# Performance work log

Measured on AMD Instinct MI355X. Metric: run time of the kernel, lower is better.

The kernel has to match this reference:

```python
import jax, jax.numpy as jnp
import numpy as np

B, LQ, LK, D = 32, 2048, 2048, 64


def setup_inputs() -> dict:
    key = jax.random.key(0)
    k1, k2, k3, k4 = jax.random.split(key, 4)
    querys = jax.random.normal(k1, (B, LQ, D), dtype=jnp.float32)
    keys = jax.random.normal(k2, (B, LK, D), dtype=jnp.float32)
    values = jax.random.normal(k3, (B, LK, D), dtype=jnp.float32)
    # valid lengths in [1, LK]
    valid_lens = jax.random.randint(k4, (B,), 1, LK + 1, dtype=jnp.int32)
    return {"querys": querys, "keys": keys, "values": values, "valid_lens": valid_lens}


def reference(querys, keys, values, valid_lens):
    d = querys.shape[-1]
    # [B, Lq, Lk] score matrix
    scores = jnp.einsum("bqd,bkd->bqk", querys, keys) / jnp.sqrt(jnp.asarray(d, querys.dtype))
    # masked softmax: key positions >= valid_len get -1e6 (as in d2l masked_softmax)
    key_pos = jnp.arange(scores.shape[-1], dtype=jnp.int32)  # [Lk]
    mask = key_pos[None, None, :] < valid_lens[:, None, None]  # [B, 1, Lk]
    scores = jnp.where(mask, scores, jnp.asarray(-1e6, scores.dtype))
    attn = jax.nn.softmax(scores, axis=-1)
    # dropout p=0.0 -> identity
    return jnp.einsum("bqk,bkd->bqd", attn, values)
```

## Files before the change

### kernel.cpp

```cpp
#include <hip/hip_runtime.h>
#include <hip/hip_bf16.h>
#include <math.h>


#define B_    32
#define LQ_   2048
#define LK_   2048
#define D_    64

typedef __attribute__((ext_vector_type(8)))  short bf16x8;
typedef __attribute__((ext_vector_type(4)))  float f32x4;
typedef __attribute__((ext_vector_type(16))) float f32x16;

static __device__ __forceinline__ unsigned pk_bf16(float a, float b) {
    __hip_bfloat162 h = __float22bfloat162_rn(float2{a, b});
    return *(unsigned*)&h;
}

__global__ __launch_bounds__(128, 2) void fa_mfma3_kernel(
    const float* __restrict__ Q, const float* __restrict__ K,
    const float* __restrict__ V, const int* __restrict__ vlen,
    float* __restrict__ O)
{
    __shared__ __align__(16) short Kl[2][64 * 64];
    __shared__ __align__(16) short Vt[2][64 * 64];

    const int tid  = threadIdx.x;
    const int wave = tid >> 6;
    const int lane = tid & 63;
    const int c31  = lane & 31;
    const int h    = lane >> 5;

    const int b  = blockIdx.y;
    const int q0 = blockIdx.x * 64 + wave * 32;
    const int vl = vlen[b];
    const int nt = (vl + 63) >> 6;

    const float qscale = 0.125f * 1.44269504088896340736f;

    unsigned qfrag[4][4];
#pragma unroll
    for (int ks = 0; ks < 4; ++ks) {
        const float* qp = Q + ((size_t)(b * LQ_ + q0 + c31)) * D_ + ks * 16 + h * 8;
        f32x4 t0 = *(const f32x4*)qp;
        f32x4 t1 = *(const f32x4*)(qp + 4);
#pragma unroll
        for (int jj = 0; jj < 2; ++jj) {
            qfrag[ks][jj]     = pk_bf16(t0[2*jj] * qscale, t0[2*jj+1] * qscale);
            qfrag[ks][jj + 2] = pk_bf16(t1[2*jj] * qscale, t1[2*jj+1] * qscale);
        }
    }

    f32x16 oacc[2];
#pragma unroll
    for (int dt = 0; dt < 2; ++dt)
#pragma unroll
        for (int r = 0; r < 16; ++r) oacc[dt][r] = 0.f;
    float mrun = -INFINITY, lrun = 0.f;

    const int skey = tid >> 1, skh = tid & 1;
    const int vkg = tid >> 4, vdg = tid & 15;

    const float* kgp = K + ((size_t)(b * LK_ + skey)) * D_ + skh * 32;
    const float* vgp = V + ((size_t)(b * LK_ + vkg * 8)) * D_ + vdg * 4;

    f32x4 kr[8], vr[8];
#pragma unroll
    for (int i = 0; i < 8; ++i) kr[i] = *(const f32x4*)(kgp + 4 * i);
#pragma unroll
    for (int i = 0; i < 8; ++i) vr[i] = *(const f32x4*)(vgp + (size_t)i * D_);

    for (int t = 0; t < nt; ++t) {
        const int k0 = t * 64;
        const int buf = t & 1;

        {
            unsigned pk32[16];
#pragma unroll
            for (int m = 0; m < 16; ++m)
                pk32[m] = pk_bf16(kr[m >> 1][2 * (m & 1)], kr[m >> 1][2 * (m & 1) + 1]);
#pragma unroll
            for (int cch = 0; cch < 4; ++cch) {
                const int pos = (skh * 4 + cch) ^ (skey & 7);
                *(bf16x8*)&Kl[buf][skey * 64 + pos * 8] = *(bf16x8*)&pk32[4 * cch];
            }
#pragma unroll
            for (int dr = 0; dr < 4; ++dr) {
                unsigned w[4];
#pragma unroll
                for (int p = 0; p < 4; ++p)
                    w[p] = pk_bf16(vr[2 * p][dr], vr[2 * p + 1][dr]);
                const int dim = vdg * 4 + dr;
                const int pos = vkg ^ (dim & 7);
                *(bf16x8*)&Vt[buf][dim * 64 + pos * 8] = *(bf16x8*)&w[0];
            }
        }
        if (t + 1 < nt) {
            const float* kn = kgp + (size_t)(k0 + 64) * D_;
            const float* vn = vgp + (size_t)(k0 + 64) * D_;
#pragma unroll
            for (int i = 0; i < 8; ++i) kr[i] = *(const f32x4*)(kn + 4 * i);
#pragma unroll
            for (int i = 0; i < 8; ++i) vr[i] = *(const f32x4*)(vn + (size_t)i * D_);
        }
        __syncthreads();

        f32x16 st[2];
#pragma unroll
        for (int s = 0; s < 2; ++s) {
#pragma unroll
            for (int r = 0; r < 16; ++r) st[s][r] = 0.f;
#pragma unroll
            for (int ks = 0; ks < 4; ++ks) {
                const int pos = (ks * 2 + h) ^ (c31 & 7);
                bf16x8 kf = *(const bf16x8*)&Kl[buf][(s * 32 + c31) * 64 + pos * 8];
                st[s] = __builtin_amdgcn_mfma_f32_32x32x16_bf16(
                    kf, *(const bf16x8*)&qfrag[ks][0], st[s], 0, 0, 0);
            }
        }

        if (k0 + 64 > vl) {
#pragma unroll
            for (int s = 0; s < 2; ++s) {
                const int base = k0 + s * 32 + 4 * h;
#pragma unroll
                for (int r = 0; r < 16; ++r) {
                    const int key = base + (r & 3) + 8 * (r >> 2);
                    if (key >= vl) st[s][r] = -1e30f;
                }
            }
        }

        float tm = st[0][0];
#pragma unroll
        for (int s = 0; s < 2; ++s)
#pragma unroll
            for (int r = 0; r < 16; ++r) tm = fmaxf(tm, st[s][r]);
        tm = fmaxf(tm, __shfl_xor(tm, 32));
        const float mnew = fmaxf(mrun, tm);
        const float corr = exp2f(mrun - mnew);
        mrun = mnew;
        float rs = 0.f;
#pragma unroll
        for (int s = 0; s < 2; ++s)
#pragma unroll
            for (int r = 0; r < 16; ++r) {
                const float p = exp2f(st[s][r] - mnew);
                st[s][r] = p;
                rs += p;
            }
        rs += __shfl_xor(rs, 32);
        lrun = lrun * corr + rs;
#pragma unroll
        for (int dt = 0; dt < 2; ++dt)
#pragma unroll
            for (int r = 0; r < 16; ++r) oacc[dt][r] *= corr;

        unsigned pk[2][8];
#pragma unroll
        for (int s = 0; s < 2; ++s)
#pragma unroll
            for (int m = 0; m < 8; ++m)
                pk[s][m] = pk_bf16(st[s][2 * m], st[s][2 * m + 1]);

#pragma unroll
        for (int kq = 0; kq < 4; ++kq) {
            const int s = kq >> 1, A4 = (kq & 1) * 4;
            unsigned p0 = pk[s][A4], p1 = pk[s][A4+1], p2 = pk[s][A4+2], p3 = pk[s][A4+3];
            unsigned xp0 = __shfl_xor((int)p0, 32);
            unsigned xp1 = __shfl_xor((int)p1, 32);
            unsigned xp2 = __shfl_xor((int)p2, 32);
            unsigned xp3 = __shfl_xor((int)p3, 32);
            unsigned pf[4];
            pf[0] = h ? xp2 : p0;
            pf[1] = h ? xp3 : p1;
            pf[2] = h ? p2  : xp0;
            pf[3] = h ? p3  : xp1;
            const bf16x8 pfr = *(const bf16x8*)&pf[0];
#pragma unroll
            for (int dt = 0; dt < 2; ++dt) {
                const int pos = (kq * 2 + h) ^ (c31 & 7);
                bf16x8 vf = *(const bf16x8*)&Vt[buf][(dt * 32 + c31) * 64 + pos * 8];
                oacc[dt] = __builtin_amdgcn_mfma_f32_32x32x16_bf16(vf, pfr, oacc[dt], 0, 0, 0);
            }
        }
    }

    const float inv = 1.f / lrun;
    float* op = O + ((size_t)(b * LQ_ + q0 + c31)) * D_;
#pragma unroll
    for (int dt = 0; dt < 2; ++dt)
#pragma unroll
        for (int g = 0; g < 4; ++g) {
            f32x4 v;
#pragma unroll
            for (int j = 0; j < 4; ++j) v[j] = oacc[dt][4 * g + j] * inv;
            *(f32x4*)(op + dt * 32 + 8 * g + 4 * h) = v;
        }
}

extern "C" void kernel_launch(void* const* d_in, const int* in_sizes, int n_in,
                              void* d_out, int out_size, void* d_ws, size_t ws_size,
                              hipStream_t stream) {
    const float* Q    = (const float*)d_in[0];
    const float* K    = (const float*)d_in[1];
    const float* V    = (const float*)d_in[2];
    const int*   vlen = (const int*)d_in[3];
    float*       O    = (float*)d_out;

    dim3 grid(LQ_ / 64, B_);
    dim3 block(128);
    fa_mfma3_kernel<<<grid, block, 0, stream>>>(Q, K, V, vlen, O);
}
```

Baseline: 171.1 us.

## Split key range across two wave groups per block and add lazy rescaling

Doubles the block to 256 threads, splitting the key tiles between two groups of waves that each handle alternating 64-key tiles into their own double-buffered LDS. The two partial softmax states are merged through shared memory at the end. Separately, the running max is updated only when a new tile max exceeds it by more than 8 (log2 domain), which skips the rescale of the accumulators most of the time. The cost is twice the LDS per block, a final cross-group reduction, extra barriers, and a lazy-rescale scheme whose bounded overflow margin must hold.

```diff
diff --git a/kernel.cpp b/kernel.cpp
--- a/kernel.cpp
+++ b/kernel.cpp
@@ -17,24 +17,28 @@
     return *(unsigned*)&h;
 }
 
-__global__ __launch_bounds__(128, 2) void fa_mfma3_kernel(
+__global__ __launch_bounds__(256, 2) void fa_mfma5_kernel(
     const float* __restrict__ Q, const float* __restrict__ K,
     const float* __restrict__ V, const int* __restrict__ vlen,
     float* __restrict__ O)
 {
-    __shared__ __align__(16) short Kl[2][64 * 64];
-    __shared__ __align__(16) short Vt[2][64 * 64];
+    __shared__ __align__(16) short Kl[2][2][64 * 64];
+    __shared__ __align__(16) short Vt[2][2][64 * 64];
 
     const int tid  = threadIdx.x;
-    const int wave = tid >> 6;
+    const int wid  = tid >> 6;
+    const int grp  = wid >> 1;
+    const int wsub = wid & 1;
     const int lane = tid & 63;
     const int c31  = lane & 31;
     const int h    = lane >> 5;
+    const int ltid = tid & 127;
 
     const int b  = blockIdx.y;
-    const int q0 = blockIdx.x * 64 + wave * 32;
+    const int q0 = blockIdx.x * 64 + wsub * 32;
     const int vl = vlen[b];
     const int nt = (vl + 63) >> 6;
+    const int ni = (nt + 1) >> 1;
 
     const float qscale = 0.125f * 1.44269504088896340736f;
 
@@ -58,23 +62,28 @@
         for (int r = 0; r < 16; ++r) oacc[dt][r] = 0.f;
     float mrun = -INFINITY, lrun = 0.f;
 
-    const int skey = tid >> 1, skh = tid & 1;
-    const int vkg = tid >> 4, vdg = tid & 15;
+    const int skey = ltid >> 1, skh = ltid & 1;
+    const int vkg = ltid >> 4, vdg = ltid & 15;
 
     const float* kgp = K + ((size_t)(b * LK_ + skey)) * D_ + skh * 32;
     const float* vgp = V + ((size_t)(b * LK_ + vkg * 8)) * D_ + vdg * 4;
 
     f32x4 kr[8], vr[8];
-#pragma unroll
-    for (int i = 0; i < 8; ++i) kr[i] = *(const f32x4*)(kgp + 4 * i);
-#pragma unroll
-    for (int i = 0; i < 8; ++i) vr[i] = *(const f32x4*)(vgp + (size_t)i * D_);
-
-    for (int t = 0; t < nt; ++t) {
-        const int k0 = t * 64;
-        const int buf = t & 1;
-
-        {
+    {
+        const size_t off = (size_t)(grp * 64) * D_;
+#pragma unroll
+        for (int i = 0; i < 8; ++i) kr[i] = *(const f32x4*)(kgp + off + 4 * i);
+#pragma unroll
+        for (int i = 0; i < 8; ++i) vr[i] = *(const f32x4*)(vgp + off + (size_t)i * D_);
+    }
+
+    for (int it = 0; it < ni; ++it) {
+        const int t   = 2 * it + grp;
+        const int k0  = t * 64;
+        const int buf = it & 1;
+        const bool active = (t < nt);
+
+        if (active) {
             unsigned pk32[16];
 #pragma unroll
             for (int m = 0; m < 16; ++m)
@@ -82,7 +91,7 @@
 #pragma unroll
             for (int cch = 0; cch < 4; ++cch) {
                 const int pos = (skh * 4 + cch) ^ (skey & 7);
-                *(bf16x8*)&Kl[buf][skey * 64 + pos * 8] = *(bf16x8*)&pk32[4 * cch];
+                *(bf16x8*)&Kl[grp][buf][skey * 64 + pos * 8] = *(bf16x8*)&pk32[4 * cch];
             }
 #pragma unroll
             for (int dr = 0; dr < 4; ++dr) {
@@ -92,18 +101,19 @@
                     w[p] = pk_bf16(vr[2 * p][dr], vr[2 * p + 1][dr]);
                 const int dim = vdg * 4 + dr;
                 const int pos = vkg ^ (dim & 7);
-                *(bf16x8*)&Vt[buf][dim * 64 + pos * 8] = *(bf16x8*)&w[0];
-            }
-        }
-        if (t + 1 < nt) {
-            const float* kn = kgp + (size_t)(k0 + 64) * D_;
-            const float* vn = vgp + (size_t)(k0 + 64) * D_;
+                *(bf16x8*)&Vt[grp][buf][dim * 64 + pos * 8] = *(bf16x8*)&w[0];
+            }
+        }
+        if (t + 2 < nt) {
+            const float* kn = kgp + (size_t)(k0 + 128) * D_;
+            const float* vn = vgp + (size_t)(k0 + 128) * D_;
 #pragma unroll
             for (int i = 0; i < 8; ++i) kr[i] = *(const f32x4*)(kn + 4 * i);
 #pragma unroll
             for (int i = 0; i < 8; ++i) vr[i] = *(const f32x4*)(vn + (size_t)i * D_);
         }
         __syncthreads();
+        if (!active) continue;
 
         f32x16 st[2];
 #pragma unroll
@@ -113,7 +123,7 @@
 #pragma unroll
             for (int ks = 0; ks < 4; ++ks) {
                 const int pos = (ks * 2 + h) ^ (c31 & 7);
-                bf16x8 kf = *(const bf16x8*)&Kl[buf][(s * 32 + c31) * 64 + pos * 8];
+                bf16x8 kf = *(const bf16x8*)&Kl[grp][buf][(s * 32 + c31) * 64 + pos * 8];
                 st[s] = __builtin_amdgcn_mfma_f32_32x32x16_bf16(
                     kf, *(const bf16x8*)&qfrag[ks][0], st[s], 0, 0, 0);
             }
@@ -137,24 +147,27 @@
 #pragma unroll
             for (int r = 0; r < 16; ++r) tm = fmaxf(tm, st[s][r]);
         tm = fmaxf(tm, __shfl_xor(tm, 32));
-        const float mnew = fmaxf(mrun, tm);
-        const float corr = exp2f(mrun - mnew);
-        mrun = mnew;
+        if (__any(tm > mrun + 8.f)) {
+            const float mnew = fmaxf(mrun, tm);
+            const float corr = exp2f(mrun - mnew);
+            lrun *= corr;
+#pragma unroll
+            for (int dt = 0; dt < 2; ++dt)
+#pragma unroll
+                for (int r = 0; r < 16; ++r) oacc[dt][r] *= corr;
+            mrun = mnew;
+        }
         float rs = 0.f;
 #pragma unroll
         for (int s = 0; s < 2; ++s)
 #pragma unroll
             for (int r = 0; r < 16; ++r) {
-                const float p = exp2f(st[s][r] - mnew);
+                const float p = exp2f(st[s][r] - mrun);
                 st[s][r] = p;
                 rs += p;
             }
         rs += __shfl_xor(rs, 32);
-        lrun = lrun * corr + rs;
-#pragma unroll
-        for (int dt = 0; dt < 2; ++dt)
-#pragma unroll
-            for (int r = 0; r < 16; ++r) oacc[dt][r] *= corr;
+        lrun += rs;
 
         unsigned pk[2][8];
 #pragma unroll
@@ -180,23 +193,52 @@
 #pragma unroll
             for (int dt = 0; dt < 2; ++dt) {
                 const int pos = (kq * 2 + h) ^ (c31 & 7);
-                bf16x8 vf = *(const bf16x8*)&Vt[buf][(dt * 32 + c31) * 64 + pos * 8];
+                bf16x8 vf = *(const bf16x8*)&Vt[grp][buf][(dt * 32 + c31) * 64 + pos * 8];
                 oacc[dt] = __builtin_amdgcn_mfma_f32_32x32x16_bf16(vf, pfr, oacc[dt], 0, 0, 0);
             }
         }
     }
 
-    const float inv = 1.f / lrun;
-    float* op = O + ((size_t)(b * LQ_ + q0 + c31)) * D_;
-#pragma unroll
-    for (int dt = 0; dt < 2; ++dt)
-#pragma unroll
-        for (int g = 0; g < 4; ++g) {
-            f32x4 v;
-#pragma unroll
-            for (int j = 0; j < 4; ++j) v[j] = oacc[dt][4 * g + j] * inv;
-            *(f32x4*)(op + dt * 32 + 8 * g + 4 * h) = v;
-        }
+    __syncthreads();
+
+    float* xO = (float*)&Kl[1][0][0];
+    float* xM = (float*)&Vt[1][0][0];
+    if (grp == 1) {
+#pragma unroll
+        for (int dt = 0; dt < 2; ++dt)
+#pragma unroll
+            for (int r = 0; r < 16; ++r) {
+                const int dim = dt * 32 + (r & 3) + 8 * (r >> 2) + 4 * h;
+                xO[wsub * 2048 + dim * 32 + c31] = oacc[dt][r];
+            }
+        if (h == 0) {
+            xM[wsub * 64 + c31]      = mrun;
+            xM[wsub * 64 + 32 + c31] = lrun;
+        }
+    }
+    __syncthreads();
+    if (grp == 0) {
+        const float m1 = xM[wsub * 64 + c31];
+        const float l1 = xM[wsub * 64 + 32 + c31];
+        const float mf = fmaxf(mrun, m1);
+        const float c0 = exp2f(mrun - mf);
+        const float c1 = exp2f(m1 - mf);
+        const float inv = 1.f / (lrun * c0 + l1 * c1);
+        float* op = O + ((size_t)(b * LQ_ + q0 + c31)) * D_;
+#pragma unroll
+        for (int dt = 0; dt < 2; ++dt)
+#pragma unroll
+            for (int g = 0; g < 4; ++g) {
+                f32x4 v;
+#pragma unroll
+                for (int j = 0; j < 4; ++j) {
+                    const int dim = dt * 32 + 8 * g + 4 * h + j;
+                    v[j] = (oacc[dt][4 * g + j] * c0 +
+                            xO[wsub * 2048 + dim * 32 + c31] * c1) * inv;
+                }
+                *(f32x4*)(op + dt * 32 + 8 * g + 4 * h) = v;
+            }
+    }
 }
 
 extern "C" void kernel_launch(void* const* d_in, const int* in_sizes, int n_in,
@@ -209,6 +251,6 @@
     float*       O    = (float*)d_out;
 
     dim3 grid(LQ_ / 64, B_);
-    dim3 block(128);
-    fa_mfma3_kernel<<<grid, block, 0, stream>>>(Q, K, V, vlen, O);
+    dim3 block(256);
+    fa_mfma5_kernel<<<grid, block, 0, stream>>>(Q, K, V, vlen, O);
 }
```

After: 171.9 us. Within noise of the previous version (+0.5%).

## Split key dimension across blocks with merge kernel and lazy rescale

Applied to the files above, without the earlier changes.

Splits each batch's key range into up to four chunks processed by separate blocks, writing partial outputs and (max, sum) stats to workspace, then merges them in a second kernel. The aim is to even out load imbalance from variable valid lengths and raise occupancy. It also adds a lazy online-softmax rescale that only updates the running max when it grows by more than 8 (log2 units). In exchange it adds substantial partial-output write and read traffic plus a second launch, and a monolithic fallback is kept for when no workspace is available.

```diff
diff --git a/kernel.cpp b/kernel.cpp
--- a/kernel.cpp
+++ b/kernel.cpp
@@ -17,10 +17,10 @@
     return *(unsigned*)&h;
 }
 
-__global__ __launch_bounds__(128, 2) void fa_mfma3_kernel(
+__global__ __launch_bounds__(128, 2) void fa_split_kernel(
     const float* __restrict__ Q, const float* __restrict__ K,
     const float* __restrict__ V, const int* __restrict__ vlen,
-    float* __restrict__ O)
+    float* __restrict__ OP, float* __restrict__ ML)
 {
     __shared__ __align__(16) short Kl[2][64 * 64];
     __shared__ __align__(16) short Vt[2][64 * 64];
@@ -32,9 +32,14 @@
     const int h    = lane >> 5;
 
     const int b  = blockIdx.y;
+    const int s  = blockIdx.z;
+    const int NS = gridDim.z;
     const int q0 = blockIdx.x * 64 + wave * 32;
     const int vl = vlen[b];
-    const int nt = (vl + 63) >> 6;
+    const int nt    = (vl + 63) >> 6;
+    const int chunk = (nt + NS - 1) / NS;
+    const int t0    = s * chunk;
+    const int t1    = min(t0 + chunk, nt);
 
     const float qscale = 0.125f * 1.44269504088896340736f;
 
@@ -42,12 +47,12 @@
 #pragma unroll
     for (int ks = 0; ks < 4; ++ks) {
         const float* qp = Q + ((size_t)(b * LQ_ + q0 + c31)) * D_ + ks * 16 + h * 8;
-        f32x4 t0 = *(const f32x4*)qp;
-        f32x4 t1 = *(const f32x4*)(qp + 4);
+        f32x4 t0v = *(const f32x4*)qp;
+        f32x4 t1v = *(const f32x4*)(qp + 4);
 #pragma unroll
         for (int jj = 0; jj < 2; ++jj) {
-            qfrag[ks][jj]     = pk_bf16(t0[2*jj] * qscale, t0[2*jj+1] * qscale);
-            qfrag[ks][jj + 2] = pk_bf16(t1[2*jj] * qscale, t1[2*jj+1] * qscale);
+            qfrag[ks][jj]     = pk_bf16(t0v[2*jj] * qscale, t0v[2*jj+1] * qscale);
+            qfrag[ks][jj + 2] = pk_bf16(t1v[2*jj] * qscale, t1v[2*jj+1] * qscale);
         }
     }
 
@@ -65,12 +70,15 @@
     const float* vgp = V + ((size_t)(b * LK_ + vkg * 8)) * D_ + vdg * 4;
 
     f32x4 kr[8], vr[8];
-#pragma unroll
-    for (int i = 0; i < 8; ++i) kr[i] = *(const f32x4*)(kgp + 4 * i);
-#pragma unroll
-    for (int i = 0; i < 8; ++i) vr[i] = *(const f32x4*)(vgp + (size_t)i * D_);
-
-    for (int t = 0; t < nt; ++t) {
+    if (t0 < t1) {
+        const size_t off = (size_t)t0 * 64 * D_;
+#pragma unroll
+        for (int i = 0; i < 8; ++i) kr[i] = *(const f32x4*)(kgp + off + 4 * i);
+#pragma unroll
+        for (int i = 0; i < 8; ++i) vr[i] = *(const f32x4*)(vgp + off + (size_t)i * D_);
+    }
+
+    for (int t = t0; t < t1; ++t) {
         const int k0 = t * 64;
         const int buf = t & 1;
 
@@ -95,7 +103,7 @@
                 *(bf16x8*)&Vt[buf][dim * 64 + pos * 8] = *(bf16x8*)&w[0];
             }
         }
-        if (t + 1 < nt) {
+        if (t + 1 < t1) {
             const float* kn = kgp + (size_t)(k0 + 64) * D_;
             const float* vn = vgp + (size_t)(k0 + 64) * D_;
 #pragma unroll
@@ -107,66 +115,69 @@
 
         f32x16 st[2];
 #pragma unroll
-        for (int s = 0; s < 2; ++s) {
-#pragma unroll
-            for (int r = 0; r < 16; ++r) st[s][r] = 0.f;
+        for (int ss = 0; ss < 2; ++ss) {
+#pragma unroll
+            for (int r = 0; r < 16; ++r) st[ss][r] = 0.f;
 #pragma unroll
             for (int ks = 0; ks < 4; ++ks) {
                 const int pos = (ks * 2 + h) ^ (c31 & 7);
-                bf16x8 kf = *(const bf16x8*)&Kl[buf][(s * 32 + c31) * 64 + pos * 8];
-                st[s] = __builtin_amdgcn_mfma_f32_32x32x16_bf16(
-                    kf, *(const bf16x8*)&qfrag[ks][0], st[s], 0, 0, 0);
+                bf16x8 kf = *(const bf16x8*)&Kl[buf][(ss * 32 + c31) * 64 + pos * 8];
+                st[ss] = __builtin_amdgcn_mfma_f32_32x32x16_bf16(
+                    kf, *(const bf16x8*)&qfrag[ks][0], st[ss], 0, 0, 0);
             }
         }
 
         if (k0 + 64 > vl) {
 #pragma unroll
-            for (int s = 0; s < 2; ++s) {
-                const int base = k0 + s * 32 + 4 * h;
+            for (int ss = 0; ss < 2; ++ss) {
+                const int base = k0 + ss * 32 + 4 * h;
 #pragma unroll
                 for (int r = 0; r < 16; ++r) {
                     const int key = base + (r & 3) + 8 * (r >> 2);
-                    if (key >= vl) st[s][r] = -1e30f;
+                    if (key >= vl) st[ss][r] = -1e30f;
                 }
             }
         }
 
         float tm = st[0][0];
 #pragma unroll
-        for (int s = 0; s < 2; ++s)
-#pragma unroll
-            for (int r = 0; r < 16; ++r) tm = fmaxf(tm, st[s][r]);
+        for (int ss = 0; ss < 2; ++ss)
+#pragma unroll
+            for (int r = 0; r < 16; ++r) tm = fmaxf(tm, st[ss][r]);
         tm = fmaxf(tm, __shfl_xor(tm, 32));
-        const float mnew = fmaxf(mrun, tm);
-        const float corr = exp2f(mrun - mnew);
-        mrun = mnew;
+        if (__any(tm > mrun + 8.f)) {
+            const float mnew = fmaxf(mrun, tm);
+            const float corr = exp2f(mrun - mnew);
+            lrun *= corr;
+#pragma unroll
+            for (int dt = 0; dt < 2; ++dt)
+#pragma unroll
+                for (int r = 0; r < 16; ++r) oacc[dt][r] *= corr;
+            mrun = mnew;
+        }
         float rs = 0.f;
 #pragma unroll
-        for (int s = 0; s < 2; ++s)
+        for (int ss = 0; ss < 2; ++ss)
 #pragma unroll
             for (int r = 0; r < 16; ++r) {
-                const float p = exp2f(st[s][r] - mnew);
-                st[s][r] = p;
+                const float p = exp2f(st[ss][r] - mrun);
+                st[ss][r] = p;
                 rs += p;
             }
         rs += __shfl_xor(rs, 32);
-        lrun = lrun * corr + rs;
-#pragma unroll
-        for (int dt = 0; dt < 2; ++dt)
-#pragma unroll
-            for (int r = 0; r < 16; ++r) oacc[dt][r] *= corr;
+        lrun += rs;
 
         unsigned pk[2][8];
 #pragma unroll
-        for (int s = 0; s < 2; ++s)
+        for (int ss = 0; ss < 2; ++ss)
 #pragma unroll
             for (int m = 0; m < 8; ++m)
-                pk[s][m] = pk_bf16(st[s][2 * m], st[s][2 * m + 1]);
+                pk[ss][m] = pk_bf16(st[ss][2 * m], st[ss][2 * m + 1]);
 
 #pragma unroll
         for (int kq = 0; kq < 4; ++kq) {
-            const int s = kq >> 1, A4 = (kq & 1) * 4;
-            unsigned p0 = pk[s][A4], p1 = pk[s][A4+1], p2 = pk[s][A4+2], p3 = pk[s][A4+3];
+            const int ss = kq >> 1, A4 = (kq & 1) * 4;
+            unsigned p0 = pk[ss][A4], p1 = pk[ss][A4+1], p2 = pk[ss][A4+2], p3 = pk[ss][A4+3];
             unsigned xp0 = __shfl_xor((int)p0, 32);
             unsigned xp1 = __shfl_xor((int)p1, 32);
             unsigned xp2 = __shfl_xor((int)p2, 32);
@@ -186,6 +197,219 @@
         }
     }
 
+    const size_t row = (size_t)s * (B_ * LQ_) + b * LQ_ + q0 + c31;
+    float* op = OP + row * D_;
+#pragma unroll
+    for (int dt = 0; dt < 2; ++dt)
+#pragma unroll
+        for (int g = 0; g < 4; ++g) {
+            f32x4 v;
+#pragma unroll
+            for (int j = 0; j < 4; ++j) v[j] = oacc[dt][4 * g + j];
+            *(f32x4*)(op + dt * 32 + 8 * g + 4 * h) = v;
+        }
+    if (h == 0)
+        *(float2*)&ML[row * 2] = float2{mrun, lrun};
+}
+
+template<int NS>
+__global__ __launch_bounds__(256) void fa_merge_kernel(
+    const float* __restrict__ OP, const float* __restrict__ ML,
+    float* __restrict__ O)
+{
+    const int g   = blockIdx.x * 256 + threadIdx.x;
+    const int row = g >> 4;
+    const int qd  = (g & 15) * 4;
+
+    float mf = -INFINITY;
+#pragma unroll
+    for (int s = 0; s < NS; ++s) {
+        float2 ml = *(const float2*)&ML[((size_t)s * (B_ * LQ_) + row) * 2];
+        mf = fmaxf(mf, ml.x);
+    }
+    float den = 0.f;
+    f32x4 acc = {0.f, 0.f, 0.f, 0.f};
+#pragma unroll
+    for (int s = 0; s < NS; ++s) {
+        const size_t srow = (size_t)s * (B_ * LQ_) + row;
+        float2 ml = *(const float2*)&ML[srow * 2];
+        const float c = exp2f(ml.x - mf);
+        den += c * ml.y;
+        f32x4 v = *(const f32x4*)&OP[srow * D_ + qd];
+        acc += v * c;
+    }
+    const float inv = 1.f / den;
+    *(f32x4*)(O + (size_t)row * D_ + qd) = acc * inv;
+}
+
+__global__ __launch_bounds__(128, 2) void fa_mono_kernel(
+    const float* __restrict__ Q, const float* __restrict__ K,
+    const float* __restrict__ V, const int* __restrict__ vlen,
+    float* __restrict__ O)
+{
+    __shared__ __align__(16) short Kl[2][64 * 64];
+    __shared__ __align__(16) short Vt[2][64 * 64];
+
+    const int tid  = threadIdx.x;
+    const int wave = tid >> 6;
+    const int lane = tid & 63;
+    const int c31  = lane & 31;
+    const int h    = lane >> 5;
+
+    const int b  = blockIdx.y;
+    const int q0 = blockIdx.x * 64 + wave * 32;
+    const int vl = vlen[b];
+    const int nt = (vl + 63) >> 6;
+
+    const float qscale = 0.125f * 1.44269504088896340736f;
+
+    unsigned qfrag[4][4];
+#pragma unroll
+    for (int ks = 0; ks < 4; ++ks) {
+        const float* qp = Q + ((size_t)(b * LQ_ + q0 + c31)) * D_ + ks * 16 + h * 8;
+        f32x4 t0 = *(const f32x4*)qp;
+        f32x4 t1 = *(const f32x4*)(qp + 4);
+#pragma unroll
+        for (int jj = 0; jj < 2; ++jj) {
+            qfrag[ks][jj]     = pk_bf16(t0[2*jj] * qscale, t0[2*jj+1] * qscale);
+            qfrag[ks][jj + 2] = pk_bf16(t1[2*jj] * qscale, t1[2*jj+1] * qscale);
+        }
+    }
+
+    f32x16 oacc[2];
+#pragma unroll
+    for (int dt = 0; dt < 2; ++dt)
+#pragma unroll
+        for (int r = 0; r < 16; ++r) oacc[dt][r] = 0.f;
+    float mrun = -INFINITY, lrun = 0.f;
+
+    const int skey = tid >> 1, skh = tid & 1;
+    const int vkg = tid >> 4, vdg = tid & 15;
+
+    const float* kgp = K + ((size_t)(b * LK_ + skey)) * D_ + skh * 32;
+    const float* vgp = V + ((size_t)(b * LK_ + vkg * 8)) * D_ + vdg * 4;
+
+    f32x4 kr[8], vr[8];
+#pragma unroll
+    for (int i = 0; i < 8; ++i) kr[i] = *(const f32x4*)(kgp + 4 * i);
+#pragma unroll
+    for (int i = 0; i < 8; ++i) vr[i] = *(const f32x4*)(vgp + (size_t)i * D_);
+
+    for (int t = 0; t < nt; ++t) {
+        const int k0 = t * 64;
+        const int buf = t & 1;
+        {
+            unsigned pk32[16];
+#pragma unroll
+            for (int m = 0; m < 16; ++m)
+                pk32[m] = pk_bf16(kr[m >> 1][2 * (m & 1)], kr[m >> 1][2 * (m & 1) + 1]);
+#pragma unroll
+            for (int cch = 0; cch < 4; ++cch) {
+                const int pos = (skh * 4 + cch) ^ (skey & 7);
+                *(bf16x8*)&Kl[buf][skey * 64 + pos * 8] = *(bf16x8*)&pk32[4 * cch];
+            }
+#pragma unroll
+            for (int dr = 0; dr < 4; ++dr) {
+                unsigned w[4];
+#pragma unroll
+                for (int p = 0; p < 4; ++p)
+                    w[p] = pk_bf16(vr[2 * p][dr], vr[2 * p + 1][dr]);
+                const int dim = vdg * 4 + dr;
+                const int pos = vkg ^ (dim & 7);
+                *(bf16x8*)&Vt[buf][dim * 64 + pos * 8] = *(bf16x8*)&w[0];
+            }
+        }
+        if (t + 1 < nt) {
+            const float* kn = kgp + (size_t)(k0 + 64) * D_;
+            const float* vn = vgp + (size_t)(k0 + 64) * D_;
+#pragma unroll
+            for (int i = 0; i < 8; ++i) kr[i] = *(const f32x4*)(kn + 4 * i);
+#pragma unroll
+            for (int i = 0; i < 8; ++i) vr[i] = *(const f32x4*)(vn + (size_t)i * D_);
+        }
+        __syncthreads();
+
+        f32x16 st[2];
+#pragma unroll
+        for (int ss = 0; ss < 2; ++ss) {
+#pragma unroll
+            for (int r = 0; r < 16; ++r) st[ss][r] = 0.f;
+#pragma unroll
+            for (int ks = 0; ks < 4; ++ks) {
+                const int pos = (ks * 2 + h) ^ (c31 & 7);
+                bf16x8 kf = *(const bf16x8*)&Kl[buf][(ss * 32 + c31) * 64 + pos * 8];
+                st[ss] = __builtin_amdgcn_mfma_f32_32x32x16_bf16(
+                    kf, *(const bf16x8*)&qfrag[ks][0], st[ss], 0, 0, 0);
+            }
+        }
+        if (k0 + 64 > vl) {
+#pragma unroll
+            for (int ss = 0; ss < 2; ++ss) {
+                const int base = k0 + ss * 32 + 4 * h;
+#pragma unroll
+                for (int r = 0; r < 16; ++r) {
+                    const int key = base + (r & 3) + 8 * (r >> 2);
+                    if (key >= vl) st[ss][r] = -1e30f;
+                }
+            }
+        }
+        float tm = st[0][0];
+#pragma unroll
+        for (int ss = 0; ss < 2; ++ss)
+#pragma unroll
+            for (int r = 0; r < 16; ++r) tm = fmaxf(tm, st[ss][r]);
+        tm = fmaxf(tm, __shfl_xor(tm, 32));
+        if (__any(tm > mrun + 8.f)) {
+            const float mnew = fmaxf(mrun, tm);
+            const float corr = exp2f(mrun - mnew);
+            lrun *= corr;
+#pragma unroll
+            for (int dt = 0; dt < 2; ++dt)
+#pragma unroll
+                for (int r = 0; r < 16; ++r) oacc[dt][r] *= corr;
+            mrun = mnew;
+        }
+        float rs = 0.f;
+#pragma unroll
+        for (int ss = 0; ss < 2; ++ss)
+#pragma unroll
+            for (int r = 0; r < 16; ++r) {
+                const float p = exp2f(st[ss][r] - mrun);
+                st[ss][r] = p;
+                rs += p;
+            }
+        rs += __shfl_xor(rs, 32);
+        lrun += rs;
+
+        unsigned pk[2][8];
+#pragma unroll
+        for (int ss = 0; ss < 2; ++ss)
+#pragma unroll
+            for (int m = 0; m < 8; ++m)
+                pk[ss][m] = pk_bf16(st[ss][2 * m], st[ss][2 * m + 1]);
+#pragma unroll
+        for (int kq = 0; kq < 4; ++kq) {
+            const int ss = kq >> 1, A4 = (kq & 1) * 4;
+            unsigned p0 = pk[ss][A4], p1 = pk[ss][A4+1], p2 = pk[ss][A4+2], p3 = pk[ss][A4+3];
+            unsigned xp0 = __shfl_xor((int)p0, 32);
+            unsigned xp1 = __shfl_xor((int)p1, 32);
+            unsigned xp2 = __shfl_xor((int)p2, 32);
+            unsigned xp3 = __shfl_xor((int)p3, 32);
+            unsigned pf[4];
+            pf[0] = h ? xp2 : p0;
+            pf[1] = h ? xp3 : p1;
+            pf[2] = h ? p2  : xp0;
+            pf[3] = h ? p3  : xp1;
+            const bf16x8 pfr = *(const bf16x8*)&pf[0];
+#pragma unroll
+            for (int dt = 0; dt < 2; ++dt) {
+                const int pos = (kq * 2 + h) ^ (c31 & 7);
+                bf16x8 vf = *(const bf16x8*)&Vt[buf][(dt * 32 + c31) * 64 + pos * 8];
+                oacc[dt] = __builtin_amdgcn_mfma_f32_32x32x16_bf16(vf, pfr, oacc[dt], 0, 0, 0);
+            }
+        }
+    }
+
     const float inv = 1.f / lrun;
     float* op = O + ((size_t)(b * LQ_ + q0 + c31)) * D_;
 #pragma unroll
@@ -208,7 +432,30 @@
     const int*   vlen = (const int*)d_in[3];
     float*       O    = (float*)d_out;
 
-    dim3 grid(LQ_ / 64, B_);
-    dim3 block(128);
-    fa_mfma3_kernel<<<grid, block, 0, stream>>>(Q, K, V, vlen, O);
+    const size_t rows = (size_t)B_ * LQ_;
+    auto need = [&](int ns) { return (size_t)ns * rows * (D_ + 2) * sizeof(float); };
+
+    int NS = 0;
+    if      (d_ws && ws_size >= need(4)) NS = 4;
+    else if (d_ws && ws_size >= need(2)) NS = 2;
+    else if (d_ws && ws_size >= need(1)) NS = 1;
+
+    if (NS == 0) {
+        dim3 grid(LQ_ / 64, B_);
+        fa_mono_kernel<<<grid, dim3(128), 0, stream>>>(Q, K, V, vlen, O);
+        return;
+    }
+
+    float* OP = (float*)d_ws;
+    float* ML = (float*)d_ws + (size_t)NS * rows * D_;
+
+    dim3 g1(LQ_ / 64, B_, NS);
+    fa_split_kernel<<<g1, dim3(128), 0, stream>>>(Q, K, V, vlen, OP, ML);
+
+    dim3 g2((unsigned)((rows * (D_ / 4)) / 256));
+    switch (NS) {
+        case 4: fa_merge_kernel<4><<<g2, dim3(256), 0, stream>>>(OP, ML, O); break;
+        case 2: fa_merge_kernel<2><<<g2, dim3(256), 0, stream>>>(OP, ML, O); break;
+        default: fa_merge_kernel<1><<<g2, dim3(256), 0, stream>>>(OP, ML, O); break;
+    }
 }
```

New measurement: 175.6 us. +2.6%, slower.
